# Kernel tuning notes

Hardware: AMD Instinct MI355X
Metric: run time of the kernel (lower is better)

The kernel has to match this reference:

```python
import jax, jax.numpy as jnp
import numpy as np

BH = 16384   # batch * n_head (B=2048, H=8)
L = 27       # seq len pinned by nn.Linear(27,27)
D = 64       # d_k, temperature = sqrt(D) = 8
N_HEAD = 8
TEMPERATURE = 8.0
A_BLEND = 0.5
B_BLEND = 0.1


def setup_inputs() -> dict:
    key = jax.random.key(0)
    kq, kk, kv, kp, kw, kb, kc = jax.random.split(key, 7)
    q = jax.random.normal(kq, (BH, L, D), dtype=jnp.float32)
    k = jax.random.normal(kk, (BH, L, D), dtype=jnp.float32)
    v = jax.random.normal(kv, (BH, L, D), dtype=jnp.float32)
    attn_pre = jax.random.normal(kp, (BH, L, L), dtype=jnp.float32)
    # causal mask (True = masked), broadcast to all BH rows; no fully-masked rows
    mask = jnp.broadcast_to(jnp.triu(jnp.ones((L, L), dtype=bool), k=1), (BH, L, L))
    lin_w = jax.random.normal(kw, (L, L), dtype=jnp.float32) * 0.1
    lin_b = jax.random.normal(kb, (L,), dtype=jnp.float32) * 0.1
    conv_w = jax.random.normal(kc, (N_HEAD, N_HEAD, L, 1), dtype=jnp.float32) * 0.05  # OIHW
    return {"q": q, "k": k, "v": v, "attn_pre": attn_pre, "mask": mask,
            "lin_w": lin_w, "lin_b": lin_b, "conv_w": conv_w}


def reference(q, k, v, attn_pre, mask, lin_w, lin_b, conv_w):
    # bmm(q, k^T) / temperature
    attn = jnp.einsum('bqd,bkd->bqk', q, k) / TEMPERATURE
    # blend with previous-layer attention
    attn = attn_pre * A_BLEND + attn * (1.0 - A_BLEND)
    # masked_fill(mask, 0) then Linear(27,27) on last axis (x @ W^T + b)
    attn_cnn = jnp.where(mask, 0.0, attn)
    attn_cnn = attn_cnn @ lin_w.T + lin_b
    # reshape to [B, n_head, Lq, Lk], conv over query axis, crop, relu
    x = attn_cnn.reshape(-1, N_HEAD, L, L)
    y = jax.lax.conv_general_dilated(
        x, conv_w, window_strides=(1, 1), padding=[(26, 26), (0, 0)],
        dimension_numbers=('NCHW', 'OIHW', 'NCHW'))
    y = jax.nn.relu(y[:, :, :L, :]).reshape(-1, L, L)
    # blend conv branch with raw scores, mask to -inf, softmax over keys
    attn = y * B_BLEND + attn * (1.0 - B_BLEND)
    attn = jnp.where(mask, -jnp.inf, attn)
    attn = jax.nn.softmax(attn, axis=2)
    # dropout is identity in eval mode
    output = jnp.einsum('bqk,bkd->bqd', attn, v)
    return output, attn
```

## Files before the change

kernel.cpp:

```cpp
#include <hip/hip_runtime.h>
#include <hip/hip_bf16.h>

typedef __hip_bfloat16 bf16;
typedef unsigned int u32;
typedef unsigned short u16;

#define NBLK 2048
#define FLAG_OFF 2484
#define OUT0 ((size_t)16384 * 27 * 64)

__device__ __forceinline__ float lo2f(u32 u) { union { u32 i; float f; } x; x.i = u << 16;          return x.f; }
__device__ __forceinline__ float hi2f(u32 u) { union { u32 i; float f; } x; x.i = u & 0xffff0000u; return x.f; }

__device__ __forceinline__ void unpack8(uint4 v, float* f) {
    f[0] = lo2f(v.x); f[1] = hi2f(v.x);
    f[2] = lo2f(v.y); f[3] = hi2f(v.y);
    f[4] = lo2f(v.z); f[5] = hi2f(v.z);
    f[6] = lo2f(v.w); f[7] = hi2f(v.w);
}

template<bool BF16>
__device__ __forceinline__ float gload(const void* p, size_t i) {
    return BF16 ? __bfloat162float(((const bf16*)p)[i]) : ((const float*)p)[i];
}

template<bool BF16>
__device__ __forceinline__ void lds_read8(const float* base, int elem, float* f) {
    if (BF16) {
        unpack8(*(const uint4*)((const u16*)base + elem), f);
    } else {
        float4 a = *(const float4*)(base + elem);
        float4 b = *(const float4*)(base + elem + 4);
        f[0] = a.x; f[1] = a.y; f[2] = a.z; f[3] = a.w;
        f[4] = b.x; f[5] = b.y; f[6] = b.z; f[7] = b.w;
    }
}

template<bool BF16>
__device__ __forceinline__ void store1(void* p, size_t i, float a) {
    if (BF16) ((bf16*)p)[i] = __float2bfloat16(a);
    else      ((float*)p)[i] = a;
}

template<bool BF16>
__device__ __forceinline__ void store2(void* p, size_t i, float a, float b) {
    if (BF16) {
        __hip_bfloat162 h2; h2.x = __float2bfloat16(a); h2.y = __float2bfloat16(b);
        *(__hip_bfloat162*)((bf16*)p + i) = h2;
    } else {
        float2 f2; f2.x = a; f2.y = b;
        *(float2*)((float*)p + i) = f2;
    }
}

template<bool BF16>
__device__ __forceinline__ int stage_dst(int idx) {
    if (BF16) {
        return (idx >> 5) * 36 + (idx & 31);
    } else {
        int col = idx & 63;
        return (idx >> 6) * 68 + col + ((col >> 5) << 2);
    }
}

__global__ __launch_bounds__(256) void detect_dtype(const u32* __restrict__ q, float* __restrict__ ws) {
    __shared__ int cnt;
    if (threadIdx.x == 0) cnt = 0;
    __syncthreads();
    int c = 0;
    for (int i = threadIdx.x; i < 512; i += 256) {
        u32 e7 = (q[i] >> 8) & 0x7F;
        if (e7 >= 0x3B && e7 <= 0x41) c++;
    }
    atomicAdd(&cnt, c);
    __syncthreads();
    if (threadIdx.x == 0) ws[FLAG_OFF] = (cnt >= 256) ? 1.0f : 0.0f;
}

template<bool BF16>
__global__ __launch_bounds__(256) void prep_weights(const void* __restrict__ lin_w,
                                                    const void* __restrict__ lin_b,
                                                    const void* __restrict__ conv_w,
                                                    float* __restrict__ ws) {
    if (ws[FLAG_OFF] != (BF16 ? 1.0f : 0.0f)) return;
    int t = threadIdx.x;
    for (int idx = t; idx < 729; idx += 256) ws[idx] = gload<BF16>(lin_w, idx);
    if (t < 27) ws[729 + t] = gload<BF16>(lin_b, t);
    for (int idx = t; idx < 1728; idx += 256) {
        int d = idx >> 6;
        int i = (idx >> 3) & 7;
        int o = idx & 7;
        ws[756 + idx] = gload<BF16>(conv_w, (o * 8 + i) * 27 + (26 - d));
    }
}

template<bool BF16>
__global__ __launch_bounds__(256) void fused_attn(const void* __restrict__ qg,
                                                  const void* __restrict__ kg,
                                                  const void* __restrict__ vg,
                                                  const void* __restrict__ apg,
                                                  const float* __restrict__ ws,
                                                  void* __restrict__ outv) {
    if (ws[FLAG_OFF] != (BF16 ? 1.0f : 0.0f)) return;

    __shared__ __align__(16) float sb[8 * 27 * 27];
    __shared__ __align__(16) float buf[7344];

    const int t = threadIdx.x;
    const int n = blockIdx.x;
    const int W32PH  = BF16 ? 864 : 1728;
    const int ROW_E  = BF16 ? 72 : 68;
    const int STG_W  = BF16 ? 1944 : 3672;
    const int KOFF_E = 54 * ROW_E;

    const float* lwf = ws;
    const float* lbf = ws + 729;
    const float* cwf = ws + 756;

    char* aout = (char*)outv + OUT0 * (BF16 ? 2 : 4);

    for (int h0 = 0; h0 < 8; h0 += 2) {
        const u32* qsrc = (const u32*)qg + (size_t)(n * 8 + h0) * W32PH;
        const u32* ksrc = (const u32*)kg + (size_t)(n * 8 + h0) * W32PH;
        u32* qb32 = (u32*)buf;
        u32* kb32 = qb32 + STG_W;
        for (int idx = t; idx < 2 * W32PH; idx += 256) {
            int dst = stage_dst<BF16>(idx);
            qb32[dst] = qsrc[idx];
            kb32[dst] = ksrc[idx];
        }
        __syncthreads();
        if (t < 162) {
            int h2 = t / 81, tl = t % 81;
            int qgr = (tl / 9) * 3, kgr = (tl % 9) * 3;
            float acc[3][3] = {};
            int qrow = (h2 * 27 + qgr) * ROW_E;
            int krow = KOFF_E + (h2 * 27 + kgr) * ROW_E;
            for (int dc = 0; dc < 8; dc++) {
                int dcoff = dc * 8 + (BF16 ? 0 : ((dc >> 2) << 2));
                float qf[3][8], kf[3][8];
                #pragma unroll
                for (int r = 0; r < 3; r++) {
                    lds_read8<BF16>(buf, qrow + r * ROW_E + dcoff, qf[r]);
                    lds_read8<BF16>(buf, krow + r * ROW_E + dcoff, kf[r]);
                }
                #pragma unroll
                for (int r = 0; r < 3; r++)
                    #pragma unroll
                    for (int c = 0; c < 3; c++)
                        #pragma unroll
                        for (int d8 = 0; d8 < 8; d8++)
                            acc[r][c] += qf[r][d8] * kf[c][d8];
            }
            int h = h0 + h2;
            size_t b = (size_t)(n * 8 + h);
            #pragma unroll
            for (int r = 0; r < 3; r++)
                #pragma unroll
                for (int c = 0; c < 3; c++) {
                    int lq = qgr + r, lk = kgr + c;
                    float apv = gload<BF16>(apg, (b * 27 + lq) * 27 + lk);
                    sb[(h * 27 + lq) * 27 + lk] = 0.5f * apv + acc[r][c] * 0.0625f;
                }
        }
        __syncthreads();
    }

    if (t < 216) {
        int h = t / 27, lq = t % 27;
        float acc[27];
        #pragma unroll
        for (int j = 0; j < 27; j++) acc[j] = lbf[j];
        const float* srow = sb + (h * 27 + lq) * 27;
        for (int i = 0; i < 27; i++) {
            float s = srow[i];
            s = (i <= lq) ? s : 0.0f;
            #pragma unroll
            for (int j = 0; j < 27; j++) acc[j] += s * lwf[j * 27 + i];
        }
        float* xrow = buf + (h * 27 + lq) * 27;
        #pragma unroll
        for (int j = 0; j < 27; j++) xrow[j] = acc[j];
    }
    __syncthreads();

    for (int r = 0; r < 3; r++) {
        int c = (r == 0) ? t : (r == 1) ? (728 - t) : (256 + t);
        bool valid = (r < 2) || (t < 217);
        int lq = c / 27;
        int e0 = __builtin_amdgcn_readlane(lq, 0);
        int e1 = __builtin_amdgcn_readlane(lq, 63);
        int bound = e0 > e1 ? e0 : e1;
        float acc8[8] = {};
        for (int d = 0; d <= bound; d++) {
            bool act = (d <= lq);
            int off = act ? (c - 27 * d) : c;
            #pragma unroll
            for (int i = 0; i < 8; i++) {
                float x = buf[i * 729 + off];
                x = act ? x : 0.0f;
                #pragma unroll
                for (int o = 0; o < 8; o++)
                    acc8[o] += cwf[(d * 8 + i) * 8 + o] * x;
            }
        }
        if (valid) {
            #pragma unroll
            for (int o = 0; o < 8; o++) {
                int sidx = o * 729 + c;
                sb[sidx] = 0.9f * sb[sidx] + 0.1f * fmaxf(acc8[o], 0.0f);
            }
        }
    }
    __syncthreads();

    if (t < 216) {
        int o = t / 27, lq = t % 27;
        float* row = sb + (o * 27 + lq) * 27;
        float m = -1e30f;
        for (int kk = 0; kk <= lq; kk++) m = fmaxf(m, row[kk]);
        float sum = 0.0f;
        for (int kk = 0; kk <= lq; kk++) {
            float e = __expf(row[kk] - m);
            row[kk] = e;
            sum += e;
        }
        float rinv = 1.0f / sum;
        size_t b = (size_t)(n * 8 + o);
        for (int kk = 0; kk < 27; kk++) {
            float p = (kk <= lq) ? row[kk] * rinv : 0.0f;
            row[kk] = p;
            store1<BF16>(aout, (b * 27 + lq) * 27 + kk, p);
        }
    }

    for (int h0 = 0; h0 < 8; h0 += 4) {
        const u32* vsrc = (const u32*)vg + (size_t)(n * 8 + h0) * W32PH;
        u32* vb = (u32*)buf;
        for (int idx = t; idx < 4 * W32PH; idx += 256) vb[stage_dst<BF16>(idx)] = vsrc[idx];
        __syncthreads();

        for (int it = t; it < 288; it += 256) {
            int hh = it / 72;
            int h = h0 + hh;
            int rem = it - hh * 72;
            int qgr = (rem >> 3) * 3;
            int dg = (rem & 7) * 8;
            int dgoff = dg + (BF16 ? 0 : ((dg >> 5) << 2));
            float acc[3][8] = {};
            const float* prow = sb + h * 729;
            int vbase = hh * 27 * ROW_E + dgoff;
            for (int kk = 0; kk < 27; kk++) {
                float vf[8];
                lds_read8<BF16>(buf, vbase + kk * ROW_E, vf);
                float p0 = prow[(qgr + 0) * 27 + kk];
                float p1 = prow[(qgr + 1) * 27 + kk];
                float p2 = prow[(qgr + 2) * 27 + kk];
                #pragma unroll
                for (int dd = 0; dd < 8; dd++) {
                    acc[0][dd] += p0 * vf[dd];
                    acc[1][dd] += p1 * vf[dd];
                    acc[2][dd] += p2 * vf[dd];
                }
            }
            size_t b = (size_t)(n * 8 + h);
            #pragma unroll
            for (int rr = 0; rr < 3; rr++)
                #pragma unroll
                for (int dd = 0; dd < 8; dd += 2)
                    store2<BF16>(outv, (b * 27 + (qgr + rr)) * 64 + dg + dd,
                                 acc[rr][dd], acc[rr][dd + 1]);
        }
        __syncthreads();
    }
}

extern "C" void kernel_launch(void* const* d_in, const int* in_sizes, int n_in,
                              void* d_out, int out_size, void* d_ws, size_t ws_size,
                              hipStream_t stream) {
    float* ws = (float*)d_ws;

    detect_dtype<<<1, 256, 0, stream>>>((const u32*)d_in[0], ws);
    prep_weights<true ><<<1, 256, 0, stream>>>(d_in[5], d_in[6], d_in[7], ws);
    prep_weights<false><<<1, 256, 0, stream>>>(d_in[5], d_in[6], d_in[7], ws);
    fused_attn<true ><<<NBLK, 256, 0, stream>>>(d_in[0], d_in[1], d_in[2], d_in[3], ws, d_out);
    fused_attn<false><<<NBLK, 256, 0, stream>>>(d_in[0], d_in[1], d_in[2], d_in[3], ws, d_out);
}
```

Baseline: 609.8 us.

## Prefetch Q/K/V chunks into registers with 16-byte loads and preload attn_pre

Global staging of Q/K and V is reorganised into register double-buffering. The next head pair's (or the next V chunk's) data is loaded as uint4 while the current chunk is being computed, then written to LDS with a padded layout. attn_pre is loaded once up front with vectorised loads, pre-scaled by 0.5 into shared memory, instead of being read with scalar gathers per output element. This is meant to hide global-load latency and widen memory transactions, at the cost of higher register pressure from up to 7 uint4 prefetch registers.

```diff
diff --git a/kernel.cpp b/kernel.cpp
--- a/kernel.cpp
+++ b/kernel.cpp
@@ -54,13 +54,10 @@
 }
 
 template<bool BF16>
-__device__ __forceinline__ int stage_dst(int idx) {
-    if (BF16) {
-        return (idx >> 5) * 36 + (idx & 31);
-    } else {
-        int col = idx & 63;
-        return (idx >> 6) * 68 + col + ((col >> 5) << 2);
-    }
+__device__ __forceinline__ int stage4_dst(int i4) {
+    if (BF16) return (i4 >> 3) * 9 + (i4 & 7);
+    int c = i4 & 15;
+    return (i4 >> 4) * 17 + c + (c >> 3);
 }
 
 __global__ __launch_bounds__(256) void detect_dtype(const u32* __restrict__ q, float* __restrict__ ws) {
@@ -108,28 +105,91 @@
 
     const int t = threadIdx.x;
     const int n = blockIdx.x;
-    const int W32PH  = BF16 ? 864 : 1728;
-    const int ROW_E  = BF16 ? 72 : 68;
-    const int STG_W  = BF16 ? 1944 : 3672;
-    const int KOFF_E = 54 * ROW_E;
+    constexpr int W32PH = BF16 ? 864 : 1728;
+    constexpr int ROW_E = BF16 ? 72 : 68;
+    constexpr int STG4  = BF16 ? 486 : 918;
+    constexpr int KOFF_E = 54 * ROW_E;
+    constexpr int NU4   = BF16 ? 864 : 1728;
+    constexpr int NREG  = BF16 ? 4 : 7;
 
     const float* lwf = ws;
     const float* lbf = ws + 729;
     const float* cwf = ws + 756;
 
     char* aout = (char*)outv + OUT0 * (BF16 ? 2 : 4);
-
-    for (int h0 = 0; h0 < 8; h0 += 2) {
-        const u32* qsrc = (const u32*)qg + (size_t)(n * 8 + h0) * W32PH;
-        const u32* ksrc = (const u32*)kg + (size_t)(n * 8 + h0) * W32PH;
-        u32* qb32 = (u32*)buf;
-        u32* kb32 = qb32 + STG_W;
-        for (int idx = t; idx < 2 * W32PH; idx += 256) {
-            int dst = stage_dst<BF16>(idx);
-            qb32[dst] = qsrc[idx];
-            kb32[dst] = ksrc[idx];
-        }
+    uint4* buf4 = (uint4*)buf;
+
+    uint4 r[NREG];
+
+    auto issue_qk = [&](int h0) {
+        const uint4* q4 = (const uint4*)((const u32*)qg + (size_t)(n * 8 + h0) * W32PH);
+        const uint4* k4 = (const uint4*)((const u32*)kg + (size_t)(n * 8 + h0) * W32PH);
+        #pragma unroll
+        for (int j = 0; j < NREG; j++) {
+            int g = t + j * 256;
+            if (g < NU4) r[j] = (g < NU4 / 2) ? q4[g] : k4[g - NU4 / 2];
+        }
+    };
+    auto write_qk = [&]() {
+        #pragma unroll
+        for (int j = 0; j < NREG; j++) {
+            int g = t + j * 256;
+            if (g < NU4) {
+                if (g < NU4 / 2) buf4[stage4_dst<BF16>(g)] = r[j];
+                else             buf4[STG4 + stage4_dst<BF16>(g - NU4 / 2)] = r[j];
+            }
+        }
+    };
+    auto issue_v = [&](int h0) {
+        const uint4* v4 = (const uint4*)((const u32*)vg + (size_t)(n * 8 + h0) * W32PH);
+        #pragma unroll
+        for (int j = 0; j < NREG; j++) {
+            int g = t + j * 256;
+            if (g < NU4) r[j] = v4[g];
+        }
+    };
+    auto write_v = [&]() {
+        #pragma unroll
+        for (int j = 0; j < NREG; j++) {
+            int g = t + j * 256;
+            if (g < NU4) buf4[stage4_dst<BF16>(g)] = r[j];
+        }
+    };
+
+    issue_qk(0);
+
+    if (BF16) {
+        const uint4* ap4 = (const uint4*)((const u16*)apg + (size_t)n * 5832);
+        #pragma unroll
+        for (int j = 0; j < 3; j++) {
+            int g = t + j * 256;
+            if (g < 729) {
+                float f[8]; unpack8(ap4[g], f);
+                float4 a = {0.5f * f[0], 0.5f * f[1], 0.5f * f[2], 0.5f * f[3]};
+                float4 b = {0.5f * f[4], 0.5f * f[5], 0.5f * f[6], 0.5f * f[7]};
+                *(float4*)(sb + g * 8)     = a;
+                *(float4*)(sb + g * 8 + 4) = b;
+            }
+        }
+    } else {
+        const float4* ap4 = (const float4*)((const float*)apg + (size_t)n * 5832);
+        #pragma unroll
+        for (int j = 0; j < 6; j++) {
+            int g = t + j * 256;
+            if (g < 1458) {
+                float4 v = ap4[g];
+                float4 w = {0.5f * v.x, 0.5f * v.y, 0.5f * v.z, 0.5f * v.w};
+                *(float4*)(sb + g * 4) = w;
+            }
+        }
+    }
+
+    for (int i = 0; i < 4; i++) {
+        write_qk();
+        if (i < 3) issue_qk(2 * (i + 1));
         __syncthreads();
+
+        const int h0 = 2 * i;
         if (t < 162) {
             int h2 = t / 81, tl = t % 81;
             int qgr = (tl / 9) * 3, kgr = (tl % 9) * 3;
@@ -140,27 +200,26 @@
                 int dcoff = dc * 8 + (BF16 ? 0 : ((dc >> 2) << 2));
                 float qf[3][8], kf[3][8];
                 #pragma unroll
-                for (int r = 0; r < 3; r++) {
-                    lds_read8<BF16>(buf, qrow + r * ROW_E + dcoff, qf[r]);
-                    lds_read8<BF16>(buf, krow + r * ROW_E + dcoff, kf[r]);
+                for (int rr = 0; rr < 3; rr++) {
+                    lds_read8<BF16>(buf, qrow + rr * ROW_E + dcoff, qf[rr]);
+                    lds_read8<BF16>(buf, krow + rr * ROW_E + dcoff, kf[rr]);
                 }
                 #pragma unroll
-                for (int r = 0; r < 3; r++)
+                for (int rr = 0; rr < 3; rr++)
                     #pragma unroll
-                    for (int c = 0; c < 3; c++)
+                    for (int cc = 0; cc < 3; cc++)
                         #pragma unroll
                         for (int d8 = 0; d8 < 8; d8++)
-                            acc[r][c] += qf[r][d8] * kf[c][d8];
+                            acc[rr][cc] += qf[rr][d8] * kf[cc][d8];
             }
             int h = h0 + h2;
-            size_t b = (size_t)(n * 8 + h);
-            #pragma unroll
-            for (int r = 0; r < 3; r++)
-                #pragma unroll
-                for (int c = 0; c < 3; c++) {
-                    int lq = qgr + r, lk = kgr + c;
-                    float apv = gload<BF16>(apg, (b * 27 + lq) * 27 + lk);
-                    sb[(h * 27 + lq) * 27 + lk] = 0.5f * apv + acc[r][c] * 0.0625f;
+            #pragma unroll
+            for (int rr = 0; rr < 3; rr++)
+                #pragma unroll
+                for (int cc = 0; cc < 3; cc++) {
+                    int lq = qgr + rr, lk = kgr + cc;
+                    int sidx = (h * 27 + lq) * 27 + lk;
+                    sb[sidx] = sb[sidx] + acc[rr][cc] * 0.0625f;
                 }
         }
         __syncthreads();
@@ -184,9 +243,9 @@
     }
     __syncthreads();
 
-    for (int r = 0; r < 3; r++) {
-        int c = (r == 0) ? t : (r == 1) ? (728 - t) : (256 + t);
-        bool valid = (r < 2) || (t < 217);
+    for (int rr = 0; rr < 3; rr++) {
+        int c = (rr == 0) ? t : (rr == 1) ? (728 - t) : (256 + t);
+        bool valid = (rr < 2) || (t < 217);
         int lq = c / 27;
         int e0 = __builtin_amdgcn_readlane(lq, 0);
         int e1 = __builtin_amdgcn_readlane(lq, 63);
@@ -213,6 +272,8 @@
         }
     }
     __syncthreads();
+
+    issue_v(0);
 
     if (t < 216) {
         int o = t / 27, lq = t % 27;
@@ -234,12 +295,12 @@
         }
     }
 
-    for (int h0 = 0; h0 < 8; h0 += 4) {
-        const u32* vsrc = (const u32*)vg + (size_t)(n * 8 + h0) * W32PH;
-        u32* vb = (u32*)buf;
-        for (int idx = t; idx < 4 * W32PH; idx += 256) vb[stage_dst<BF16>(idx)] = vsrc[idx];
-        __syncthreads();
-
+    write_v();
+    issue_v(4);
+    __syncthreads();
+
+    for (int ch = 0; ch < 2; ch++) {
+        const int h0 = ch * 4;
         for (int it = t; it < 288; it += 256) {
             int hh = it / 72;
             int h = h0 + hh;
@@ -271,7 +332,11 @@
                     store2<BF16>(outv, (b * 27 + (qgr + rr)) * 64 + dg + dd,
                                  acc[rr][dd], acc[rr][dd + 1]);
         }
-        __syncthreads();
+        if (ch == 0) {
+            __syncthreads();
+            write_v();
+            __syncthreads();
+        }
     }
 }
 
```

Result: slower. 652.2 us (+7.0%).
